# Optimization experiments

Hardware: AMD Instinct MI355X
Metric: run time of the kernel (lower is better)

The kernel has to match this reference:

```python
import jax, jax.numpy as jnp
import numpy as np

NEG = -1e30  # effective -inf, safe under fp32


def setup_inputs() -> dict:
    key = jax.random.key(0)
    k1, k2, k3 = jax.random.split(key, 3)
    T, B, C, L = 2000, 512, 29, 150  # C = num_classes + num_replabels = 28 + 1
    inputs = jax.random.normal(k1, (T, B, C), dtype=jnp.float32)
    transitions = jax.random.normal(k2, (C + 1, C), dtype=jnp.float32) * 0.1
    targets = jax.random.randint(k3, (B, L), 0, C, dtype=jnp.int32)
    return {"inputs": inputs, "transitions": transitions, "targets": targets}


def _asg_loss(inputs, transitions, targets):
    # inputs: [T, B, C] unnormalized emissions (time-major, as fed to the module)
    # transitions: [C+1, C]; row 0 = start scores, transitions[1+c, p] = score(p -> c)
    # targets: [B, L] int labels (replabel-packed), values in [0, C)
    T, B, C = inputs.shape
    L = targets.shape[1]
    start = transitions[0]          # [C]
    trans = transitions[1:]         # [C, C]; trans[next, prev]

    # ---- denominator: log-sum-exp over all paths in the fully connected lattice ----
    alpha0 = inputs[0] + start[None, :]                                   # [B, C]
    def den_step(alpha, e_t):
        # alpha[b, p] -> logsumexp_p(alpha[b, p] + trans[c, p]) per next-class c
        a = jax.nn.logsumexp(alpha[:, None, :] + trans[None, :, :], axis=-1)
        return e_t + a, None
    alphaT, _ = jax.lax.scan(den_step, alpha0, inputs[1:])
    log_den = jax.nn.logsumexp(alphaT, axis=-1)                           # [B]

    # ---- numerator: forced alignment over the target chain with self-loops ----
    idx = jnp.broadcast_to(targets[None, :, :], (T, B, L))
    e_y = jnp.take_along_axis(inputs, idx, axis=2)                        # [T, B, L]
    stay_t = trans[targets, targets]                                      # [B, L] self-loop
    move_t = trans[targets[:, 1:], targets[:, :-1]]                       # [B, L-1] y_{l-1}->y_l
    move_t = jnp.concatenate([jnp.zeros((B, 1), inputs.dtype), move_t], axis=1)
    l_is0 = jnp.arange(L) == 0
    num0 = jnp.where(l_is0[None, :], start[targets[:, 0]][:, None] + e_y[0], NEG)
    def num_step(alpha, e_t):
        shifted = jnp.pad(alpha[:, :-1], ((0, 0), (1, 0)), constant_values=NEG)
        a = jnp.logaddexp(alpha + stay_t, shifted + move_t)
        return e_t + a, None
    alphaL, _ = jax.lax.scan(num_step, num0, e_y[1:])
    log_num = alphaL[:, -1]                                               # [B]

    # loss_b = logZ_full - logZ_forced_align; 'mean' reduction over batch
    return jnp.mean(log_den - log_num)


def reference(inputs, transitions, targets):
    return _asg_loss(inputs, transitions, targets)
```

## Files before the change

### kernel.cpp

```cpp
#include <hip/hip_runtime.h>

static constexpr int Tn = 2000;
static constexpr int Bn = 512;
static constexpr int Cn = 29;
static constexpr int Ln = 150;
static constexpr float LOG2E_F = 1.4426950408889634f;
static constexpr float LN2_F   = 0.6931471805599453f;
static constexpr float NEGV    = -1e30f;

static constexpr int WS_DEN_F = 0;
static constexpr int WS_NUM_F = 2 * 512 * 32;
static constexpr int WS_NUM_B = 2 * 512 * 32 + 512 * 160;

static constexpr int NSEG = 8;
static constexpr int SEGL = 250;

typedef float  f32x16 __attribute__((ext_vector_type(16)));
typedef float  f32x4  __attribute__((ext_vector_type(4)));
typedef float  f32x2  __attribute__((ext_vector_type(2)));
typedef __bf16 bf16x8 __attribute__((ext_vector_type(8)));
typedef unsigned int u32x4 __attribute__((ext_vector_type(4)));

#if __has_builtin(__builtin_amdgcn_exp2f)
#define FEXP2(x) __builtin_amdgcn_exp2f(x)
#else
#define FEXP2(x) exp2f(x)
#endif
#if __has_builtin(__builtin_amdgcn_logf)
#define FLOG2(x) __builtin_amdgcn_logf(x)
#else
#define FLOG2(x) log2f(x)
#endif

__device__ __forceinline__ int exp_of(float x) {
    return ((__float_as_int(x) >> 23) & 255) - 127;
}
__device__ __forceinline__ float pow2i(int e) {
    return __int_as_float((e + 127) << 23);
}
__device__ __forceinline__ unsigned short f2bf_rne(float x) {
    unsigned u = __float_as_uint(x);
    u += 0x7fffu + ((u >> 16) & 1u);
    return (unsigned short)(u >> 16);
}
__device__ __forceinline__ unsigned cvtpk_bf16(float lo, float hi) {
    unsigned r;
    asm("v_cvt_pk_bf16_f32 %0, %1, %2" : "=v"(r) : "v"(lo), "v"(hi));
    return r;
}
__device__ __forceinline__ void xswap32(unsigned &a, unsigned &b) {
#if __has_builtin(__builtin_amdgcn_permlane32_swap)
    auto r = __builtin_amdgcn_permlane32_swap(a, b, false, false);
    a = r[0]; b = r[1];
#else
    unsigned pa = (unsigned)__shfl_xor((int)a, 32);
    unsigned pb = (unsigned)__shfl_xor((int)b, 32);
    bool hb = (threadIdx.x & 32) != 0;
    unsigned na = hb ? pb : a;
    unsigned nb = hb ? b : pa;
    a = na; b = nb;
#endif
}
__device__ __forceinline__ void packDtoB(const float* W, bf16x8 &B1, bf16x8 &B2) {
    unsigned pk[8];
#pragma unroll
    for (int q = 0; q < 8; ++q) pk[q] = cvtpk_bf16(W[2 * q], W[2 * q + 1]);
    xswap32(pk[0], pk[2]); xswap32(pk[1], pk[3]);
    xswap32(pk[4], pk[6]); xswap32(pk[5], pk[7]);
    B1 = __builtin_bit_cast(bf16x8, u32x4{pk[0], pk[1], pk[2], pk[3]});
    B2 = __builtin_bit_cast(bf16x8, u32x4{pk[4], pk[5], pk[6], pk[7]});
}
__device__ __forceinline__ void renorm16(float* W, float &Sacc) {
    float m = W[0];
#pragma unroll
    for (int r = 1; r < 16; ++r) m = fmaxf(m, W[r]);
#pragma unroll
    for (int sh = 1; sh <= 32; sh <<= 1) m = fmaxf(m, __shfl_xor(m, sh));
    int g = exp_of(m);
    float iv = pow2i(-g);
    f32x2 iv2 = {iv, iv};
    f32x2* W2 = (f32x2*)W;
#pragma unroll
    for (int j = 0; j < 8; ++j) W2[j] = W2[j] * iv2;
    Sacc += (float)g;
}

__global__ __launch_bounds__(512)
void asg_scan(const float* __restrict__ inp, const float* __restrict__ tr,
              const int* __restrict__ tg, float* __restrict__ ws)
{
    const int tid = threadIdx.x;
    const int bid = blockIdx.x;
    const int wv  = __builtin_amdgcn_readfirstlane(tid >> 6);

    __shared__ unsigned am[NSEG][32][20];
    __shared__ float uring[NSEG][8][32];
    __shared__ float scl[NSEG];

    if (bid >= 128) {
        const int lane = tid & 63;
        const int col  = lane & 31;
        const int hi   = lane >> 5;
        const int b    = bid - 128;
        const size_t BC = (size_t)Bn * Cn;

        unsigned aw[8];
#pragma unroll
        for (int p = 0; p < 8; ++p) {
            int kb = (p >> 2) * 16 + 8 * hi + (p & 3) * 2;
            unsigned short lo = 0, hh = 0;
            if (col < Cn) {
                if (kb < Cn)     lo = f2bf_rne(FEXP2(LOG2E_F * tr[(1 + col) * Cn + kb]));
                if (kb + 1 < Cn) hh = f2bf_rne(FEXP2(LOG2E_F * tr[(1 + col) * Cn + kb + 1]));
            }
            aw[p] = (unsigned)lo | ((unsigned)hh << 16);
        }
        const bf16x8 A1 = __builtin_bit_cast(bf16x8, u32x4{aw[0], aw[1], aw[2], aw[3]});
        const bf16x8 A2 = __builtin_bit_cast(bf16x8, u32x4{aw[4], aw[5], aw[6], aw[7]});

        f32x16 z;
#pragma unroll
        for (int r = 0; r < 16; ++r) z[r] = 0.f;

        const int start = 1 + SEGL * wv;
        const int cnt   = min(SEGL, Tn - start);

        const int cofs = min(col, Cn - 1);
        const float* bbase = inp + (size_t)b * Cn;
        auto ldrow = [&](int t) { return (bbase + (size_t)t * BC)[cofs]; };

        float er[8];
#pragma unroll
        for (int p = 0; p < 8; ++p) er[p] = ldrow(min(start + p, Tn - 1));

        if (lane < 32) {
            uring[wv][0][col] = FEXP2(LOG2E_F * er[0]);
            uring[wv][1][col] = FEXP2(LOG2E_F * er[1]);
        }

        float W[16];
#pragma unroll
        for (int r = 0; r < 16; ++r) {
            int row = (r & 3) + 8 * (r >> 2) + 4 * hi;
            W[r] = (row == col) ? 1.0f : 0.0f;
        }
        float Sacc = 0.f;

        int s = 0;
        for (; s + 8 <= cnt; s += 8) {
#pragma unroll
            for (int u = 0; u < 8; ++u) {
                er[u] = ldrow(min(start + s + u + 8, Tn - 1));
                float un = FEXP2(LOG2E_F * er[(u + 2) & 7]);
                if (lane < 32) uring[wv][(u + 2) & 7][col] = un;
                f32x4 uu0 = *(const f32x4*)&uring[wv][u][4 * hi];
                f32x4 uu1 = *(const f32x4*)&uring[wv][u][8 + 4 * hi];
                f32x4 uu2 = *(const f32x4*)&uring[wv][u][16 + 4 * hi];
                f32x4 uu3 = *(const f32x4*)&uring[wv][u][24 + 4 * hi];
                bf16x8 B1, B2;
                packDtoB(W, B1, B2);
                f32x16 d = __builtin_amdgcn_mfma_f32_32x32x16_bf16(A1, B1, z, 0, 0, 0);
                d = __builtin_amdgcn_mfma_f32_32x32x16_bf16(A2, B2, d, 0, 0, 0);
                f32x2* W2 = (f32x2*)W;
                W2[0] = f32x2{d[0],  d[1]}  * f32x2{uu0.x, uu0.y};
                W2[1] = f32x2{d[2],  d[3]}  * f32x2{uu0.z, uu0.w};
                W2[2] = f32x2{d[4],  d[5]}  * f32x2{uu1.x, uu1.y};
                W2[3] = f32x2{d[6],  d[7]}  * f32x2{uu1.z, uu1.w};
                W2[4] = f32x2{d[8],  d[9]}  * f32x2{uu2.x, uu2.y};
                W2[5] = f32x2{d[10], d[11]} * f32x2{uu2.z, uu2.w};
                W2[6] = f32x2{d[12], d[13]} * f32x2{uu3.x, uu3.y};
                W2[7] = f32x2{d[14], d[15]} * f32x2{uu3.z, uu3.w};
                if (u == 7) renorm16(W, Sacc);
            }
        }
        {
            const int rem = cnt - s;
#pragma unroll
            for (int u = 0; u < 2; ++u) {
                if (u < rem) {
                    f32x4 uu0 = *(const f32x4*)&uring[wv][u][4 * hi];
                    f32x4 uu1 = *(const f32x4*)&uring[wv][u][8 + 4 * hi];
                    f32x4 uu2 = *(const f32x4*)&uring[wv][u][16 + 4 * hi];
                    f32x4 uu3 = *(const f32x4*)&uring[wv][u][24 + 4 * hi];
                    bf16x8 B1, B2;
                    packDtoB(W, B1, B2);
                    f32x16 d = __builtin_amdgcn_mfma_f32_32x32x16_bf16(A1, B1, z, 0, 0, 0);
                    d = __builtin_amdgcn_mfma_f32_32x32x16_bf16(A2, B2, d, 0, 0, 0);
#pragma unroll
                    for (int r = 0; r < 16; ++r) {
                        f32x4 uq = (r < 4) ? uu0 : (r < 8) ? uu1 : (r < 12) ? uu2 : uu3;
                        W[r] = d[r] * uq[r & 3];
                    }
                }
            }
            renorm16(W, Sacc);
        }

        {
            unsigned short* s16 = (unsigned short*)am[wv];
#pragma unroll
            for (int r = 0; r < 16; ++r) {
                int row = (r & 3) + 8 * (r >> 2) + 4 * hi;
                s16[row * 40 + col] = f2bf_rne(W[r]);
            }
        }
        if (lane == 0) scl[wv] = Sacc;
        __syncthreads();

        auto lds_mul = [&](int Ls, int Rs, float* Wo) {
            u32x4 a0 = *(const u32x4*)&am[Ls][col][4 * hi];
            u32x4 a1 = *(const u32x4*)&am[Ls][col][8 + 4 * hi];
            bf16x8 LA1 = __builtin_bit_cast(bf16x8, a0);
            bf16x8 LA2 = __builtin_bit_cast(bf16x8, a1);
            const unsigned short* r16 = (const unsigned short*)am[Rs];
            unsigned pk[8];
#pragma unroll
            for (int q = 0; q < 8; ++q) {
                int ra = ((2 * q) & 3) + 8 * ((2 * q) >> 2) + 4 * hi;
                pk[q] = (unsigned)r16[ra * 40 + col] |
                        ((unsigned)r16[(ra + 1) * 40 + col] << 16);
            }
            xswap32(pk[0], pk[2]); xswap32(pk[1], pk[3]);
            xswap32(pk[4], pk[6]); xswap32(pk[5], pk[7]);
            bf16x8 B1 = __builtin_bit_cast(bf16x8, u32x4{pk[0], pk[1], pk[2], pk[3]});
            bf16x8 B2 = __builtin_bit_cast(bf16x8, u32x4{pk[4], pk[5], pk[6], pk[7]});
            f32x16 d = __builtin_amdgcn_mfma_f32_32x32x16_bf16(LA1, B1, z, 0, 0, 0);
            d = __builtin_amdgcn_mfma_f32_32x32x16_bf16(LA2, B2, d, 0, 0, 0);
#pragma unroll
            for (int r = 0; r < 16; ++r) Wo[r] = d[r];
        };
        auto store_mat = [&](int slot, const float* Wo) {
            unsigned short* s16 = (unsigned short*)am[slot];
#pragma unroll
            for (int r = 0; r < 16; ++r) {
                int row = (r & 3) + 8 * (r >> 2) + 4 * hi;
                s16[row * 40 + col] = f2bf_rne(Wo[r]);
            }
        };

        if (wv < 4) {
            float Wq[16];
            lds_mul(2 * wv + 1, 2 * wv, Wq);
            float Sg = scl[2 * wv] + scl[2 * wv + 1];
            renorm16(Wq, Sg);
            store_mat(2 * wv, Wq);
            if (lane == 0) scl[2 * wv] = Sg;
        }
        __syncthreads();
        if (wv < 2) {
            float Wq[16];
            lds_mul(4 * wv + 2, 4 * wv, Wq);
            float Sg = scl[4 * wv] + scl[4 * wv + 2];
            renorm16(Wq, Sg);
            store_mat(4 * wv, Wq);
            if (lane == 0) scl[4 * wv] = Sg;
        }
        __syncthreads();
        if (wv == 0) {
            float Wq[16];
            lds_mul(4, 0, Wq);
            const float Stot = scl[0] + scl[4];
            float a0v = 0.f;
            if (col < Cn)
                a0v = FEXP2(LOG2E_F * (inp[(size_t)b * Cn + col] + tr[col]));
            float ssum = 0.f;
#pragma unroll
            for (int r = 0; r < 16; ++r) ssum += Wq[r];
            float t = ssum * a0v;
#pragma unroll
            for (int sh = 1; sh <= 32; sh <<= 1) t += __shfl_xor(t, sh);
            if (lane == 0) ws[WS_DEN_F + b] = FLOG2(t) + Stot;
        }
    } else {
        const int nid = bid * 8 + wv;
        const int dir = nid >> 9;
        const int b   = nid & 511;
        const int k   = tid & 63;
        const int* tb = tg + b * Ln;

        const int l0 = 3 * k, l1 = 3 * k + 1, l2 = 3 * k + 2;
        const int t0i = (l0 < Ln) ? tb[l0] : 0;
        const int t1i = (l1 < Ln) ? tb[l1] : 0;
        const int t2i = (l2 < Ln) ? tb[l2] : 0;
        const float S0 = FEXP2(LOG2E_F * tr[(1 + t0i) * Cn + t0i]);
        const float S1 = FEXP2(LOG2E_F * tr[(1 + t1i) * Cn + t1i]);
        const float S2 = FEXP2(LOG2E_F * tr[(1 + t2i) * Cn + t2i]);
        const float M0 = (l0 >= 1 && l0 < Ln)
                         ? FEXP2(LOG2E_F * tr[(1 + t0i) * Cn + tb[l0 - 1]]) : 0.f;
        const float M1 = (l1 < Ln) ? FEXP2(LOG2E_F * tr[(1 + t1i) * Cn + t0i]) : 0.f;
        const float M2 = (l2 < Ln) ? FEXP2(LOG2E_F * tr[(1 + t2i) * Cn + t1i]) : 0.f;

        float w0 = 0.f, w1 = 0.f, w2 = 0.f;
        if (dir == 0) {
            if (k == 0) w0 = FEXP2(LOG2E_F * (tr[t0i] + inp[(size_t)b * Cn + t0i]));
        } else {
            if (k == 49) w2 = 1.f;
        }
        int   sE  = 0;
        float m0x = M0;
        float fdn = 1.f;
        int   pgx = 0, psp = 0;

        const size_t BC = (size_t)Bn * Cn;
        const int cofs = min(k, Cn - 1);
        const float* bbase = inp + (size_t)b * Cn;
        auto ldrow = [&](int t) { return (bbase + (size_t)t * BC)[cofs]; };
        const int t0 = dir ? (Tn - 1) : 1;
        const int dt = dir ? -1 : 1;
        const int steps = dir ? 1000 : 999;

        float ue0[4], ue1[4], ue2[4], rr[4];
#pragma unroll
        for (int u = 0; u < 4; ++u) {
            float ux = FEXP2(LOG2E_F * ldrow(t0 + u * dt));
            ue0[u] = __shfl(ux, t0i);
            ue1[u] = __shfl(ux, t1i);
            ue2[u] = __shfl(ux, t2i);
        }

        for (int s = 0; s < steps; s += 4) {
#pragma unroll
            for (int u = 0; u < 4; ++u)
                rr[u] = ldrow(t0 + (s + 4 + u) * dt);
#pragma unroll
            for (int u = 0; u < 4; ++u) {
                if (s + u < steps) {
                    if (u == 1) {
                        float rs = pow2i(-pgx);
                        w0 *= rs; w1 *= rs; w2 *= rs; sE += pgx;
                        int df = psp - sE;
                        df = max(-126, min(56, df));
                        float fx = pow2i(df);
                        m0x = M0 * fx; fdn = fx;
                    }
                    if (dir == 0) {
                        float sh = __shfl_up(w2, 1);
                        sh = (k == 0) ? 0.f : sh;
                        float nn0 = ue0[u] * fmaf(w0, S0, sh * m0x);
                        float nn1 = ue1[u] * fmaf(w1, S1, w0 * M1);
                        float nn2 = ue2[u] * fmaf(w2, S2, w1 * M2);
                        w0 = nn0; w1 = nn1; w2 = nn2;
                    } else {
                        float q0 = w0 * ue0[u], q1 = w1 * ue1[u], q2 = w2 * ue2[u];
                        float mn = __shfl_down(q0 * M0, 1);
                        w0 = fmaf(q0, S0, q1 * M1);
                        w1 = fmaf(q1, S1, q2 * M2);
                        w2 = fmaf(q2, S2, mn * fdn);
                    }
                    if (u == 3) {
                        float mxn = fmaxf(fmaxf(w0, w1), w2);
                        pgx = (mxn > 0.f) ? exp_of(mxn) : 0;
                        int sp = sE + pgx;
                        psp = dir ? __shfl_down(sp, 1) : __shfl_up(sp, 1);
                    }
                }
            }
#pragma unroll
            for (int u = 0; u < 4; ++u) {
                float ux = FEXP2(LOG2E_F * rr[u]);
                ue0[u] = __shfl(ux, t0i);
                ue1[u] = __shfl(ux, t1i);
                ue2[u] = __shfl(ux, t2i);
            }
        }
        const float fsE = (float)sE;
        const int base = (dir ? WS_NUM_B : WS_NUM_F) + b * 160;
        if (l0 < Ln)     ws[base + l0]     = (w0 > 0.f) ? FLOG2(w0) + fsE : NEGV;
        if (l0 + 1 < Ln) ws[base + l0 + 1] = (w1 > 0.f) ? FLOG2(w1) + fsE : NEGV;
        if (l0 + 2 < Ln) ws[base + l0 + 2] = (w2 > 0.f) ? FLOG2(w2) + fsE : NEGV;
    }
}

__global__ __launch_bounds__(512)
void asg_combine(const float* __restrict__ ws, float* __restrict__ out)
{
    __shared__ float red[512];
    const int b = threadIdx.x;

    const float ld = ws[WS_DEN_F + b];

    const float* nf = ws + WS_NUM_F + b * 160;
    const float* nb = ws + WS_NUM_B + b * 160;
    float vm2 = -3.0e38f;
    for (int l = 0; l < Ln; ++l) vm2 = fmaxf(vm2, nf[l] + nb[l]);
    float sum2 = 0.f;
    for (int l = 0; l < Ln; ++l) sum2 += FEXP2(nf[l] + nb[l] - vm2);
    float ln = vm2 + FLOG2(sum2);

    red[b] = ld - ln;
    __syncthreads();
    for (int off = 256; off > 0; off >>= 1) {
        if (b < off) red[b] += red[b + off];
        __syncthreads();
    }
    if (b == 0) out[0] = red[0] * (LN2_F / 512.0f);
}

extern "C" void kernel_launch(void* const* d_in, const int* in_sizes, int n_in,
                              void* d_out, int out_size, void* d_ws, size_t ws_size,
                              hipStream_t stream)
{
    const float* inp = (const float*)d_in[0];
    const float* tr  = (const float*)d_in[1];
    const int*   tg  = (const int*)d_in[2];
    float* out = (float*)d_out;
    float* ws  = (float*)d_ws;

    hipLaunchKernelGGL(asg_scan,    dim3(640), dim3(512), 0, stream, inp, tr, tg, ws);
    hipLaunchKernelGGL(asg_combine, dim3(1),   dim3(512), 0, stream, ws, out);
}
```

Baseline: 220.2 us.

## Pack two batch items per wavefront in numerator scan with five states per lane

The numerator forward/backward scan now gives each batch item 32 lanes holding five lattice states each, so one 64-lane wavefront serves two batch items instead of one item spread over 50 lanes at three states each. This halves the number of numerator wavefronts and blocks (128 down to 64), and the grid shrinks from 640 to 576 blocks. The cost is a longer serial dependency chain per lane (five states per step), more registers, and more shuffles per time step.

After: 261.8 us. +18.9%, slower.

```diff
diff --git a/kernel.cpp b/kernel.cpp
--- a/kernel.cpp
+++ b/kernel.cpp
@@ -97,11 +97,11 @@
     __shared__ float uring[NSEG][8][32];
     __shared__ float scl[NSEG];
 
-    if (bid >= 128) {
+    if (bid >= 64) {
         const int lane = tid & 63;
         const int col  = lane & 31;
         const int hi   = lane >> 5;
-        const int b    = bid - 128;
+        const int b    = bid - 64;
         const size_t BC = (size_t)Bn * Cn;
 
         unsigned aw[8];
@@ -272,50 +272,55 @@
             if (lane == 0) ws[WS_DEN_F + b] = FLOG2(t) + Stot;
         }
     } else {
-        const int nid = bid * 8 + wv;
-        const int dir = nid >> 9;
-        const int b   = nid & 511;
-        const int k   = tid & 63;
+        const int w   = bid * 8 + wv;
+        const int dir = w >> 8;
+        const int pr  = w & 255;
+        const int lk  = tid & 63;
+        const int k   = lk & 31;
+        const int grp = lk >> 5;
+        const int b   = 2 * pr + grp;
+        const int gb  = grp << 5;
         const int* tb = tg + b * Ln;
-
-        const int l0 = 3 * k, l1 = 3 * k + 1, l2 = 3 * k + 2;
-        const int t0i = (l0 < Ln) ? tb[l0] : 0;
-        const int t1i = (l1 < Ln) ? tb[l1] : 0;
-        const int t2i = (l2 < Ln) ? tb[l2] : 0;
-        const float S0 = FEXP2(LOG2E_F * tr[(1 + t0i) * Cn + t0i]);
-        const float S1 = FEXP2(LOG2E_F * tr[(1 + t1i) * Cn + t1i]);
-        const float S2 = FEXP2(LOG2E_F * tr[(1 + t2i) * Cn + t2i]);
-        const float M0 = (l0 >= 1 && l0 < Ln)
-                         ? FEXP2(LOG2E_F * tr[(1 + t0i) * Cn + tb[l0 - 1]]) : 0.f;
-        const float M1 = (l1 < Ln) ? FEXP2(LOG2E_F * tr[(1 + t1i) * Cn + t0i]) : 0.f;
-        const float M2 = (l2 < Ln) ? FEXP2(LOG2E_F * tr[(1 + t2i) * Cn + t1i]) : 0.f;
-
-        float w0 = 0.f, w1 = 0.f, w2 = 0.f;
+        const bool act = (k < 30);
+
+        int ti[5];
+#pragma unroll
+        for (int j = 0; j < 5; ++j) ti[j] = act ? tb[5 * k + j] : 0;
+        float S[5], M[5];
+#pragma unroll
+        for (int j = 0; j < 5; ++j)
+            S[j] = act ? FEXP2(LOG2E_F * tr[(1 + ti[j]) * Cn + ti[j]]) : 0.f;
+        M[0] = (act && k >= 1) ? FEXP2(LOG2E_F * tr[(1 + ti[0]) * Cn + tb[5 * k - 1]]) : 0.f;
+#pragma unroll
+        for (int j = 1; j < 5; ++j)
+            M[j] = act ? FEXP2(LOG2E_F * tr[(1 + ti[j]) * Cn + ti[j - 1]]) : 0.f;
+
+        float w0 = 0.f, w1 = 0.f, w2 = 0.f, w3 = 0.f, w4 = 0.f;
         if (dir == 0) {
-            if (k == 0) w0 = FEXP2(LOG2E_F * (tr[t0i] + inp[(size_t)b * Cn + t0i]));
+            if (k == 0) w0 = FEXP2(LOG2E_F * (tr[ti[0]] + inp[(size_t)b * Cn + ti[0]]));
         } else {
-            if (k == 49) w2 = 1.f;
+            if (k == 29) w4 = 1.f;
         }
         int   sE  = 0;
-        float m0x = M0;
+        float m0x = M[0];
         float fdn = 1.f;
         int   pgx = 0, psp = 0;
 
         const size_t BC = (size_t)Bn * Cn;
-        const int cofs = min(k, Cn - 1);
-        const float* bbase = inp + (size_t)b * Cn;
-        auto ldrow = [&](int t) { return (bbase + (size_t)t * BC)[cofs]; };
+        const int bo = b * Cn + min(k, Cn - 1);
+        auto ldrow = [&](int t) { return inp[(size_t)t * BC + bo]; };
         const int t0 = dir ? (Tn - 1) : 1;
         const int dt = dir ? -1 : 1;
         const int steps = dir ? 1000 : 999;
-
-        float ue0[4], ue1[4], ue2[4], rr[4];
+        const int g0 = gb + ti[0], g1 = gb + ti[1], g2 = gb + ti[2],
+                  g3 = gb + ti[3], g4 = gb + ti[4];
+
+        float ue0[4], ue1[4], ue2[4], ue3[4], ue4[4], rr[4];
 #pragma unroll
         for (int u = 0; u < 4; ++u) {
             float ux = FEXP2(LOG2E_F * ldrow(t0 + u * dt));
-            ue0[u] = __shfl(ux, t0i);
-            ue1[u] = __shfl(ux, t1i);
-            ue2[u] = __shfl(ux, t2i);
+            ue0[u] = __shfl(ux, g0); ue1[u] = __shfl(ux, g1); ue2[u] = __shfl(ux, g2);
+            ue3[u] = __shfl(ux, g3); ue4[u] = __shfl(ux, g4);
         }
 
         for (int s = 0; s < steps; s += 4) {
@@ -327,28 +332,34 @@
                 if (s + u < steps) {
                     if (u == 1) {
                         float rs = pow2i(-pgx);
-                        w0 *= rs; w1 *= rs; w2 *= rs; sE += pgx;
+                        w0 *= rs; w1 *= rs; w2 *= rs; w3 *= rs; w4 *= rs; sE += pgx;
                         int df = psp - sE;
                         df = max(-126, min(56, df));
                         float fx = pow2i(df);
-                        m0x = M0 * fx; fdn = fx;
+                        m0x = M[0] * fx; fdn = fx;
                     }
                     if (dir == 0) {
-                        float sh = __shfl_up(w2, 1);
+                        float sh = __shfl_up(w4, 1);
                         sh = (k == 0) ? 0.f : sh;
-                        float nn0 = ue0[u] * fmaf(w0, S0, sh * m0x);
-                        float nn1 = ue1[u] * fmaf(w1, S1, w0 * M1);
-                        float nn2 = ue2[u] * fmaf(w2, S2, w1 * M2);
-                        w0 = nn0; w1 = nn1; w2 = nn2;
+                        float n0 = ue0[u] * fmaf(w0, S[0], sh * m0x);
+                        float n1 = ue1[u] * fmaf(w1, S[1], w0 * M[1]);
+                        float n2 = ue2[u] * fmaf(w2, S[2], w1 * M[2]);
+                        float n3 = ue3[u] * fmaf(w3, S[3], w2 * M[3]);
+                        float n4 = ue4[u] * fmaf(w4, S[4], w3 * M[4]);
+                        w0 = n0; w1 = n1; w2 = n2; w3 = n3; w4 = n4;
                     } else {
-                        float q0 = w0 * ue0[u], q1 = w1 * ue1[u], q2 = w2 * ue2[u];
-                        float mn = __shfl_down(q0 * M0, 1);
-                        w0 = fmaf(q0, S0, q1 * M1);
-                        w1 = fmaf(q1, S1, q2 * M2);
-                        w2 = fmaf(q2, S2, mn * fdn);
+                        float q0 = w0 * ue0[u], q1 = w1 * ue1[u], q2 = w2 * ue2[u],
+                              q3 = w3 * ue3[u], q4 = w4 * ue4[u];
+                        float mn = __shfl_down(q0 * M[0], 1);
+                        mn = (k >= 29) ? 0.f : mn;
+                        w0 = fmaf(q0, S[0], q1 * M[1]);
+                        w1 = fmaf(q1, S[1], q2 * M[2]);
+                        w2 = fmaf(q2, S[2], q3 * M[3]);
+                        w3 = fmaf(q3, S[3], q4 * M[4]);
+                        w4 = fmaf(q4, S[4], mn * fdn);
                     }
                     if (u == 3) {
-                        float mxn = fmaxf(fmaxf(w0, w1), w2);
+                        float mxn = fmaxf(fmaxf(fmaxf(w0, w1), fmaxf(w2, w3)), w4);
                         pgx = (mxn > 0.f) ? exp_of(mxn) : 0;
                         int sp = sE + pgx;
                         psp = dir ? __shfl_down(sp, 1) : __shfl_up(sp, 1);
@@ -358,16 +369,18 @@
 #pragma unroll
             for (int u = 0; u < 4; ++u) {
                 float ux = FEXP2(LOG2E_F * rr[u]);
-                ue0[u] = __shfl(ux, t0i);
-                ue1[u] = __shfl(ux, t1i);
-                ue2[u] = __shfl(ux, t2i);
+                ue0[u] = __shfl(ux, g0); ue1[u] = __shfl(ux, g1); ue2[u] = __shfl(ux, g2);
+                ue3[u] = __shfl(ux, g3); ue4[u] = __shfl(ux, g4);
             }
         }
         const float fsE = (float)sE;
         const int base = (dir ? WS_NUM_B : WS_NUM_F) + b * 160;
-        if (l0 < Ln)     ws[base + l0]     = (w0 > 0.f) ? FLOG2(w0) + fsE : NEGV;
-        if (l0 + 1 < Ln) ws[base + l0 + 1] = (w1 > 0.f) ? FLOG2(w1) + fsE : NEGV;
-        if (l0 + 2 < Ln) ws[base + l0 + 2] = (w2 > 0.f) ? FLOG2(w2) + fsE : NEGV;
+        if (act) {
+            float wa[5] = {w0, w1, w2, w3, w4};
+#pragma unroll
+            for (int j = 0; j < 5; ++j)
+                ws[base + 5 * k + j] = (wa[j] > 0.f) ? FLOG2(wa[j]) + fsE : NEGV;
+        }
     }
 }
 
@@ -406,6 +419,6 @@
     float* out = (float*)d_out;
     float* ws  = (float*)d_ws;
 
-    hipLaunchKernelGGL(asg_scan,    dim3(640), dim3(512), 0, stream, inp, tr, tg, ws);
+    hipLaunchKernelGGL(asg_scan,    dim3(576), dim3(512), 0, stream, inp, tr, tg, ws);
     hipLaunchKernelGGL(asg_combine, dim3(1),   dim3(512), 0, stream, ws, out);
 }
```
